# Performance work log

Measured on AMD Instinct MI355X. Metric: run time of the kernel, lower is better.

## Reference

```python
import jax, jax.numpy as jnp
import numpy as np

N = 80000      # nodes (spots)
D = 1000       # input_dim (genes)
E = 1280000    # edges (avg degree 16)
FH1, FH2 = 64, 16
GH1, GH2 = 64, 16
K = 10         # dec_cluster_n
ALPHA = 1.0
MASK = int(0.8 * N)
BN_EPS = 1e-3


def _xavier(key, shape):
    fan_in, fan_out = shape[0], shape[1]
    lim = jnp.sqrt(6.0 / (fan_in + fan_out))
    return jax.random.uniform(key, shape, jnp.float32, -lim, lim)


def setup_inputs() -> dict:
    key = jax.random.key(0)
    ks = jax.random.split(key, 32)
    x = jax.random.normal(ks[0], (N, D), jnp.float32)
    edge_rows = jax.random.randint(ks[1], (E,), 0, N, jnp.int32)
    edge_cols = jax.random.randint(ks[2], (E,), 0, N, jnp.int32)
    edge_vals = jax.random.uniform(ks[3], (E,), jnp.float32)
    mask_nodes = jax.random.permutation(ks[4], N)[:MASK].astype(jnp.int32)
    enc_mask_token = 0.02 * jax.random.normal(ks[5], (1, D), jnp.float32)
    # encoder L1: Linear + BatchNorm (eval: running stats)
    W1 = _xavier(ks[6], (D, FH1)); b1 = jnp.zeros((FH1,), jnp.float32)
    g1 = jnp.ones((FH1,), jnp.float32); be1 = jnp.zeros((FH1,), jnp.float32)
    rm1 = 0.1 * jax.random.normal(ks[7], (FH1,), jnp.float32)
    rv1 = 0.5 + jax.random.uniform(ks[8], (FH1,), jnp.float32)
    # encoder L2
    W2 = _xavier(ks[9], (FH1, FH2)); b2 = jnp.zeros((FH2,), jnp.float32)
    g2 = jnp.ones((FH2,), jnp.float32); be2 = jnp.zeros((FH2,), jnp.float32)
    rm2 = 0.1 * jax.random.normal(ks[10], (FH2,), jnp.float32)
    rv2 = 0.5 + jax.random.uniform(ks[11], (FH2,), jnp.float32)
    # GCN weights
    Wgc1 = _xavier(ks[12], (FH2, GH1))
    Wgc2 = _xavier(ks[13], (GH1, GH2))
    Wgc3 = _xavier(ks[14], (GH1, GH2))
    Wdec = _xavier(ks[15], (GH2 + FH2, D))
    cluster_layer = jax.random.normal(ks[16], (K, GH2 + FH2), jnp.float32) * jnp.sqrt(2.0 / (K + GH2 + FH2))
    return dict(x=x, edge_rows=edge_rows, edge_cols=edge_cols, edge_vals=edge_vals,
                mask_nodes=mask_nodes, enc_mask_token=enc_mask_token,
                W1=W1, b1=b1, g1=g1, be1=be1, rm1=rm1, rv1=rv1,
                W2=W2, b2=b2, g2=g2, be2=be2, rm2=rm2, rv2=rv2,
                Wgc1=Wgc1, Wgc2=Wgc2, Wgc3=Wgc3, Wdec=Wdec,
                cluster_layer=cluster_layer)


def _bn_eval(h, g, b, rm, rv):
    return (h - rm) * (g * jax.lax.rsqrt(rv + BN_EPS)) + b


def _spmm(rows, cols, vals, dense):
    # sparse adj [N,N] @ dense [N,F]
    return jax.ops.segment_sum(vals[:, None] * dense[cols], rows, num_segments=N)


def _l2norm(v):
    n = jnp.sqrt(jnp.sum(v * v, axis=-1, keepdims=True))
    return v / jnp.maximum(n, 1e-12)


def reference(x, edge_rows, edge_cols, edge_vals, mask_nodes, enc_mask_token,
              W1, b1, g1, be1, rm1, rv1, W2, b2, g2, be2, rm2, rv2,
              Wgc1, Wgc2, Wgc3, Wdec, cluster_layer):
    # encoding_mask_noise: add mask token to masked nodes (eval: dropout off)
    out_x = x.at[mask_nodes].add(enc_mask_token[0])
    # dense encoder (Linear -> BN(eval) -> ELU; dropout off)
    h = jax.nn.elu(_bn_eval(out_x @ W1 + b1, g1, be1, rm1, rv1))
    feat_x = jax.nn.elu(_bn_eval(h @ W2 + b2, g2, be2, rm2, rv2))
    # GCN layers: mm then spmm
    hidden1 = jax.nn.relu(_spmm(edge_rows, edge_cols, edge_vals, feat_x @ Wgc1))
    mu = _spmm(edge_rows, edge_cols, edge_vals, hidden1 @ Wgc2)
    logvar = _spmm(edge_rows, edge_cols, edge_vals, hidden1 @ Wgc3)
    gnn_z = mu  # eval-mode reparameterize
    z = jnp.concatenate([feat_x, gnn_z], axis=1)  # [N, 32]
    de_feat = _spmm(edge_rows, edge_cols, edge_vals, z @ Wdec)  # identity act
    # student-t cluster soft assignments
    d2 = jnp.sum(jnp.square(z[:, None, :] - cluster_layer[None, :, :]), axis=2)  # [N,K]
    q = 1.0 / (1.0 + d2 / ALPHA)
    q = q ** ((ALPHA + 1.0) / 2.0)
    q = q / jnp.sum(q, axis=1, keepdims=True)
    # sce loss on masked nodes
    x_init = out_x[mask_nodes]
    x_rec = de_feat[mask_nodes]
    loss = jnp.mean((1.0 - jnp.sum(_l2norm(x_rec) * _l2norm(x_init), axis=-1)) ** 3)
    return (z, mu, logvar, de_feat, q, feat_x, gnn_z, loss)
```

## Files before the change

kernel.cpp:

```cpp
#include <hip/hip_runtime.h>
#include <hip/hip_bf16.h>
#include <math.h>

#define Nn 80000
#define Dd 1000
#define Ee 1280000
#define MM 64000
#define NT 32

typedef __attribute__((ext_vector_type(8))) short bf16x8;
typedef __attribute__((ext_vector_type(4))) float f32x4;

__device__ inline unsigned short f2bf(float f){
  union { float f; unsigned u; } c; c.f = f;
  unsigned u = c.u;
  u += 0x7FFFu + ((u >> 16) & 1u);
  return (unsigned short)(u >> 16);
}
__device__ inline float bf2f(unsigned short s){
  return __uint_as_float(((unsigned)s) << 16);
}

__device__ __forceinline__ void gload16(const void* g, void* l){
  __builtin_amdgcn_global_load_lds(
      (const __attribute__((address_space(1))) void*)g,
      (__attribute__((address_space(3))) void*)l, 16, 0, 0);
}

__device__ __forceinline__ bf16x8 cvt8(f32x4 a, f32x4 b){
  union { __hip_bfloat162 h; unsigned u; } c0, c1, c2, c3;
  c0.h = __float22bfloat162_rn(make_float2(a.x, a.y));
  c1.h = __float22bfloat162_rn(make_float2(a.z, a.w));
  c2.h = __float22bfloat162_rn(make_float2(b.x, b.y));
  c3.h = __float22bfloat162_rn(make_float2(b.z, b.w));
  union { unsigned u[4]; bf16x8 v; } r;
  r.u[0] = c0.u; r.u[1] = c1.u; r.u[2] = c2.u; r.u[3] = c3.u;
  return r.v;
}

__global__ __launch_bounds__(256) void k_init(const float* __restrict__ W1,
    const float* __restrict__ Wdec, const float* __restrict__ token,
    unsigned short* __restrict__ Wim, unsigned short* __restrict__ WdT2,
    float* __restrict__ tw, int* __restrict__ flags, int* __restrict__ deg,
    float* __restrict__ loss)
{
  int i = blockIdx.x*256 + threadIdx.x;
  if (i < 131072){
    int t   = i >> 12;
    int rem = i & 4095;
    int c   = rem >> 5;
    int pos = rem & 31;
    int slot = pos >> 3;
    int j    = pos & 7;
    int u    = slot ^ (c & 3);
    int k    = t*32 + u*8 + j;
    float v = 0.f;
    if (c < 96 && k < Dd) v = (c < 64) ? W1[k*64 + c] : Wdec[(size_t)(c-64)*Dd + k];
    Wim[i] = f2bf(v);
  }
  unsigned t1 = (unsigned)(i - 131072);
  if (t1 < 32768u){
    int col = t1 >> 5, k = t1 & 31;
    WdT2[t1] = (col < Dd) ? f2bf(Wdec[(size_t)k*Dd + col]) : (unsigned short)0;
  }
  if (i < Nn){ flags[i] = 0; deg[i] = 0; }
  if (i == 0) *loss = 0.f;
  unsigned u3 = (unsigned)(i - 163840);
  if (u3 < 6208u){
    int j = u3 >> 6, l = u3 & 63;
    float s = 0.f;
    if (j < 64){ for (int k = l; k < Dd; k += 64) s += token[k]*W1[k*64 + j]; }
    else if (j < 96){ const float* wr = Wdec + (size_t)(j-64)*Dd;
                      for (int k = l; k < Dd; k += 64) s += token[k]*wr[k]; }
    else { for (int k = l; k < Dd; k += 64) s += token[k]*token[k]; }
    #pragma unroll
    for (int o = 32; o; o >>= 1) s += __shfl_down(s, o);
    if (l == 0) tw[j] = s;
  }
}

__global__ __launch_bounds__(256) void k_fillb(const int* __restrict__ rows,
    const int* __restrict__ cols, const float* __restrict__ vals,
    const int* __restrict__ mask, int* __restrict__ flags,
    int* __restrict__ deg, int2* __restrict__ buck, int lo, int hi)
{
  int i = blockIdx.x*256 + threadIdx.x;
  if (lo == 0 && i < MM) flags[mask[i]] = 1;
  if (i < Ee){
    int r = rows[i];
    if (r >= lo && r < hi){
      int s = atomicAdd(&deg[r], 1);
      if (s < 64){
        int2 pr; pr.x = cols[i]; pr.y = __float_as_int(vals[i]);
        buck[((size_t)r << 6) + s] = pr;
      }
    }
  }
}

__global__ __launch_bounds__(256, 3) void k_gemm1(
    const float* __restrict__ x, const unsigned short* __restrict__ Wim,
    const int* __restrict__ flags, const float* __restrict__ tw,
    const float* __restrict__ token,
    const float* __restrict__ b1, const float* __restrict__ g1,
    const float* __restrict__ be1, const float* __restrict__ rm1,
    const float* __restrict__ rv1, const float* __restrict__ W2,
    const float* __restrict__ b2, const float* __restrict__ g2,
    const float* __restrict__ be2, const float* __restrict__ rm2,
    const float* __restrict__ rv2, float* __restrict__ fx,
    float* __restrict__ wx, float* __restrict__ sii_node)
{
  __shared__ char smem[53248];
  float* tokL = (float*)(smem + 49152);
  const int tid  = threadIdx.x;
  const int lane = tid & 63;
  const int wave = tid >> 6;
  const int wm = wave >> 1, wn = wave & 1;
  const int l15 = lane & 15, kg = lane >> 4;
  const int swz = l15 & 7;
  const int row0 = blockIdx.x * 128;

  for (int i = tid; i < 1024; i += 256) tokL[i] = (i < Dd) ? token[i] : 0.f;
  __syncthreads();

  auto stage = [&](int t, char* Ab, char* Bb){
    int k0 = t*32;
    #pragma unroll
    for (int j = 0; j < 4; ++j){
      int s = (wave*4 + j)*64 + lane;
      int r = s >> 3, u = s & 7;
      int col = k0 + ((u ^ (r & 7)) << 2);
      if (col > 996) col = 996;
      gload16(x + (size_t)(row0 + r)*Dd + col, Ab + (wave*4 + j)*1024);
    }
    const char* wim = (const char*)Wim + (size_t)t*8192;
    #pragma unroll
    for (int j = 0; j < 2; ++j){
      int ch = wave*2 + j;
      gload16(wim + ch*1024 + lane*16, Bb + ch*1024);
    }
  };

  stage(0, smem,         smem + 32768);
  stage(1, smem + 16384, smem + 40960);

  const f32x4 zero4 = {0.f,0.f,0.f,0.f};
  f32x4 acc[4][3];
  #pragma unroll
  for (int i = 0; i < 4; ++i){ acc[i][0]=zero4; acc[i][1]=zero4; acc[i][2]=zero4; }
  float sx2[4] = {0.f,0.f,0.f,0.f};
  float sxt[4] = {0.f,0.f,0.f,0.f};

  #pragma unroll 2
  for (int t = 0; t < NT; ++t){
    if (t < NT-1) asm volatile("s_waitcnt vmcnt(6)" ::: "memory");
    else          asm volatile("s_waitcnt vmcnt(0)" ::: "memory");
    __builtin_amdgcn_s_barrier();
    __builtin_amdgcn_sched_barrier(0);

    const char* Ab = smem + (t&1)*16384;
    const char* Bb = smem + 32768 + (t&1)*8192;
    const int k0 = t*32;

    f32x4 tk0 = *(const f32x4*)(tokL + k0 + kg*8);
    f32x4 tk1 = *(const f32x4*)(tokL + k0 + kg*8 + 4);

    bf16x8 bfr[3];
    #pragma unroll
    for (int ni = 0; ni < 3; ++ni){
      int c = wn*48 + ni*16 + l15;
      bfr[ni] = *(const bf16x8*)(Bb + c*64 + ((kg ^ (c & 3)) << 4));
    }
    bool kv = (k0 + kg*8) <= 992;
    #pragma unroll
    for (int mi = 0; mi < 4; ++mi){
      int r = wm*64 + mi*16 + l15;
      f32x4 xa = *(const f32x4*)(Ab + r*128 + (((2*kg  ) ^ swz) << 4));
      f32x4 xb = *(const f32x4*)(Ab + r*128 + (((2*kg+1) ^ swz) << 4));
      if (wn == 0 && kv){
        sx2[mi] += xa.x*xa.x + xa.y*xa.y + xa.z*xa.z + xa.w*xa.w
                 + xb.x*xb.x + xb.y*xb.y + xb.z*xb.z + xb.w*xb.w;
        sxt[mi] += xa.x*tk0.x + xa.y*tk0.y + xa.z*tk0.z + xa.w*tk0.w
                 + xb.x*tk1.x + xb.y*tk1.y + xb.z*tk1.z + xb.w*tk1.w;
      }
      bf16x8 af = cvt8(xa, xb);
      acc[mi][0] = __builtin_amdgcn_mfma_f32_16x16x32_bf16(af, bfr[0], acc[mi][0], 0, 0, 0);
      acc[mi][1] = __builtin_amdgcn_mfma_f32_16x16x32_bf16(af, bfr[1], acc[mi][1], 0, 0, 0);
      acc[mi][2] = __builtin_amdgcn_mfma_f32_16x16x32_bf16(af, bfr[2], acc[mi][2], 0, 0, 0);
    }

    __builtin_amdgcn_sched_barrier(0);
    __builtin_amdgcn_s_barrier();
    if (t + 2 < NT)
      stage(t+2, smem + (t&1)*16384, smem + 32768 + (t&1)*8192);
  }

  float stt = tw[96];
  if (wn == 0){
    #pragma unroll
    for (int mi = 0; mi < 4; ++mi){
      float a2 = sx2[mi]; a2 += __shfl_xor(a2, 16); a2 += __shfl_xor(a2, 32);
      float at = sxt[mi]; at += __shfl_xor(at, 16); at += __shfl_xor(at, 32);
      if (lane < 16){
        int row = row0 + wm*64 + mi*16 + lane;
        float fl = flags[row] ? 1.f : 0.f;
        sii_node[row] = a2 + fl*(2.f*at + stt);
      }
    }
  }

  float flv[4][4];
  #pragma unroll
  for (int mi = 0; mi < 4; ++mi)
    #pragma unroll
    for (int r4 = 0; r4 < 4; ++r4)
      flv[mi][r4] = flags[row0 + wm*64 + mi*16 + (lane>>4)*4 + r4] ? 1.f : 0.f;

  float* Hs  = (float*)smem;
  float* W2s = (float*)(smem + 36864);
  for (int i = tid; i < 1024; i += 256) W2s[i] = W2[i];

  #pragma unroll
  for (int ni = 0; ni < 3; ++ni){
    int n = wn*48 + ni*16 + l15;
    float twn = tw[n];
    if (n < 64){
      float bb = b1[n], rmv = rm1[n];
      float scv = g1[n]*rsqrtf(rv1[n] + 1e-3f), bev = be1[n];
      #pragma unroll
      for (int mi = 0; mi < 4; ++mi){
        #pragma unroll
        for (int r4 = 0; r4 < 4; ++r4){
          int lrow = wm*64 + mi*16 + (lane>>4)*4 + r4;
          float v = (acc[mi][ni][r4] + flv[mi][r4]*twn + bb - rmv)*scv + bev;
          v = (v > 0.f) ? v : expm1f(v);
          Hs[lrow*66 + n] = v;
        }
      }
    } else {
      int j = n - 64;
      #pragma unroll
      for (int mi = 0; mi < 4; ++mi){
        #pragma unroll
        for (int r4 = 0; r4 < 4; ++r4){
          int lrow = wm*64 + mi*16 + (lane>>4)*4 + r4;
          wx[(size_t)(row0 + lrow)*32 + j] = acc[mi][ni][r4] + flv[mi][r4]*twn;
        }
      }
    }
  }
  __syncthreads();

  {
    int j = tid & 15;
    float pb = b2[j], prm = rm2[j];
    float psc = g2[j]*rsqrtf(rv2[j] + 1e-3f), pbe = be2[j];
    int rb = (tid >> 4) * 8;
    #pragma unroll
    for (int rr = 0; rr < 8; ++rr){
      int r = rb + rr;
      float a = pb;
      #pragma unroll
      for (int k = 0; k < 64; ++k) a += Hs[r*66 + k]*W2s[k*16 + j];
      float v = (a - prm)*psc + pbe;
      v = (v > 0.f) ? v : expm1f(v);
      fx[(size_t)(row0 + r)*16 + j] = v;
    }
  }
}

template<bool WITH_H1>
__global__ __launch_bounds__(256) void k_spmm16(const int* __restrict__ deg,
    const int2* __restrict__ buck, const float* __restrict__ in,
    float* __restrict__ out, const float* __restrict__ Wgc1,
    unsigned short* __restrict__ h1b)
{
  __shared__ float Ws[1024];
  if (WITH_H1){
    for (int t = threadIdx.x; t < 1024; t += 256) Ws[t] = Wgc1[t];
    __syncthreads();
  }
  int row = blockIdx.x*16 + (threadIdx.x >> 4);
  int l = threadIdx.x & 15;
  int d = deg[row]; if (d > 64) d = 64;
  const int2* bp = buck + ((size_t)row << 6);
  float acc = 0.f;
  for (int p = 0; p < d; ++p){
    int2 ce = bp[p];
    acc += __int_as_float(ce.y) * in[(size_t)ce.x*16 + l];
  }
  out[(size_t)row*16 + l] = acc;
  if (WITH_H1){
    float h0=0.f, h1=0.f, h2=0.f, h3=0.f;
    #pragma unroll
    for (int k = 0; k < 16; ++k){
      float av = __shfl(acc, k, 16);
      const float* wp = &Ws[k*64 + l*4];
      h0 += av*wp[0]; h1 += av*wp[1]; h2 += av*wp[2]; h3 += av*wp[3];
    }
    ushort4 pk;
    pk.x = f2bf(fmaxf(h0, 0.f)); pk.y = f2bf(fmaxf(h1, 0.f));
    pk.z = f2bf(fmaxf(h2, 0.f)); pk.w = f2bf(fmaxf(h3, 0.f));
    *reinterpret_cast<ushort4*>(&h1b[(size_t)row*64 + l*4]) = pk;
  }
}

__global__ __launch_bounds__(256) void k_gcn2(const int* __restrict__ deg,
    const int2* __restrict__ buck, const unsigned short* __restrict__ h1b,
    const float* __restrict__ Wgc2, const float* __restrict__ Wgc3,
    const float* __restrict__ fx, const float* __restrict__ cl,
    float* __restrict__ z, float* __restrict__ mu,
    float* __restrict__ lv, float* __restrict__ gz, float* __restrict__ q)
{
  __shared__ float ah[16][65];
  __shared__ float Ws[2048];
  __shared__ float cls[320];
  __shared__ float zs[16][33];
  __shared__ float qv[16][10];
  int t = threadIdx.x;
  for (int i = t; i < 1024; i += 256){ Ws[i] = Wgc2[i]; Ws[1024 + i] = Wgc3[i]; }
  for (int i = t; i < 320; i += 256) cls[i] = cl[i];
  const int wave = t >> 6, lane = t & 63;
  const int row0 = blockIdx.x*16;
  #pragma unroll
  for (int rr = 0; rr < 4; ++rr){
    int lr = wave*4 + rr;
    int row = row0 + lr;
    int d = deg[row]; if (d > 64) d = 64;
    const int2* bp = buck + ((size_t)row << 6);
    float acc = 0.f;
    for (int p = 0; p < d; ++p){
      int2 ce = bp[p];
      acc += __int_as_float(ce.y) * bf2f(h1b[(size_t)ce.x*64 + lane]);
    }
    ah[lr][lane] = acc;
  }
  __syncthreads();
  {
    int r = t >> 4, j = t & 15;
    const float* ar = ah[r];
    float m = 0.f, l = 0.f;
    #pragma unroll 16
    for (int k = 0; k < 64; ++k){
      float a = ar[k];
      m += a*Ws[k*16 + j];
      l += a*Ws[1024 + k*16 + j];
    }
    size_t grow = (size_t)(row0 + r);
    mu[grow*16 + j] = m;
    gz[grow*16 + j] = m;
    z[grow*32 + 16 + j] = m;
    zs[r][16 + j] = m;
    lv[grow*16 + j] = l;
    float v = fx[grow*16 + j];
    z[grow*32 + j] = v;
    zs[r][j] = v;
  }
  __syncthreads();
  if (t < 160){
    int r = t / 10, c = t - r*10;
    float d2 = 0.f;
    #pragma unroll
    for (int k = 0; k < 32; ++k){ float d = zs[r][k] - cls[c*32 + k]; d2 += d*d; }
    qv[r][c] = 1.f/(1.f + d2);
  }
  __syncthreads();
  if (t < 160){
    int r = t / 10, c = t - r*10;
    float ss = 0.f;
    #pragma unroll
    for (int cc = 0; cc < 10; ++cc) ss += qv[r][cc];
    q[(size_t)(row0 + r)*10 + c] = qv[r][c]/ss;
  }
}

__global__ __launch_bounds__(256) void k_dec(const float* __restrict__ afx,
    const float* __restrict__ amu, const unsigned short* __restrict__ WdT2,
    const float* __restrict__ wx, const float* __restrict__ sii_node,
    const int* __restrict__ flags, float* __restrict__ de,
    float* __restrict__ loss)
{
  __shared__ float stg[4][16][68];
  __shared__ float bsum[4];
  const int lane = threadIdx.x & 63;
  const int wave = threadIdx.x >> 6;
  const int r0 = blockIdx.x*64 + wave*16;
  const int kg = lane >> 4;
  const int l15 = lane & 15;
  const int row = r0 + l15;
  const float* asrc = (kg < 2) ? (afx + (size_t)row*16 + kg*8)
                               : (amu + (size_t)row*16 + (kg-2)*8);
  f32x4 a0 = *reinterpret_cast<const f32x4*>(asrc);
  f32x4 a1 = *reinterpret_cast<const f32x4*>(asrc + 4);
  bf16x8 af = cvt8(a0, a1);
  const float* wsrc = wx + (size_t)row*32 + kg*8;
  f32x4 w0 = *reinterpret_cast<const f32x4*>(wsrc);
  f32x4 w1 = *reinterpret_cast<const f32x4*>(wsrc + 4);
  float sri = a0.x*w0.x + a0.y*w0.y + a0.z*w0.z + a0.w*w0.w
            + a1.x*w1.x + a1.y*w1.y + a1.z*w1.z + a1.w*w1.w;

  const f32x4 zero4 = {0.f,0.f,0.f,0.f};
  float sq = 0.f;
  float (*S)[68] = stg[wave];
  const int srow = lane >> 4;
  const int scol = l15*4;

  for (int g = 0; g < 16; ++g){
    int c0 = g*64;
    #pragma unroll
    for (int j = 0; j < 4; ++j){
      int cb = c0 + j*16;
      bf16x8 bf = *reinterpret_cast<const bf16x8*>(&WdT2[(size_t)(cb + l15)*32 + kg*8]);
      f32x4 d = __builtin_amdgcn_mfma_f32_16x16x32_bf16(bf, af, zero4, 0, 0, 0);
      sq += d[0]*d[0] + d[1]*d[1] + d[2]*d[2] + d[3]*d[3];
      *reinterpret_cast<f32x4*>(&S[l15][j*16 + kg*4]) = d;
    }
    asm volatile("s_waitcnt lgkmcnt(0)" ::: "memory");
    __builtin_amdgcn_sched_barrier(0);
    #pragma unroll
    for (int sub = 0; sub < 4; ++sub){
      int lr = sub*4 + srow;
      int cc = c0 + scol;
      if (cc < Dd){
        f32x4 v = *reinterpret_cast<const f32x4*>(&S[lr][scol]);
        *reinterpret_cast<f32x4*>(&de[(size_t)(r0 + lr)*Dd + cc]) = v;
      }
    }
    __builtin_amdgcn_sched_barrier(0);
    asm volatile("s_waitcnt lgkmcnt(0)" ::: "memory");
  }
  sq  += __shfl_xor(sq, 16);  sq  += __shfl_xor(sq, 32);
  sri += __shfl_xor(sri, 16); sri += __shfl_xor(sri, 32);
  float tval = 0.f;
  if (kg == 0){
    float nr = fmaxf(sqrtf(sq), 1e-12f);
    float ni = fmaxf(sqrtf(sii_node[row]), 1e-12f);
    float tt = 1.f - sri/(nr*ni);
    tval = flags[row] ? tt*tt*tt : 0.f;
  }
  #pragma unroll
  for (int o = 1; o < 16; o <<= 1) tval += __shfl_xor(tval, o);
  if (lane == 0) bsum[wave] = tval;
  __syncthreads();
  if (threadIdx.x == 0)
    atomicAdd(loss, (bsum[0] + bsum[1] + bsum[2] + bsum[3]) * (1.f/MM));
}

extern "C" void kernel_launch(void* const* d_in, const int* in_sizes, int n_in,
                              void* d_out, int out_size, void* d_ws, size_t ws_size,
                              hipStream_t stream)
{
  const float* x     = (const float*)d_in[0];
  const int*   erow  = (const int*)  d_in[1];
  const int*   ecol  = (const int*)  d_in[2];
  const float* evls  = (const float*)d_in[3];
  const int*   mask  = (const int*)  d_in[4];
  const float* token = (const float*)d_in[5];
  const float* W1  = (const float*)d_in[6];
  const float* b1  = (const float*)d_in[7];
  const float* g1  = (const float*)d_in[8];
  const float* be1 = (const float*)d_in[9];
  const float* rm1 = (const float*)d_in[10];
  const float* rv1 = (const float*)d_in[11];
  const float* W2  = (const float*)d_in[12];
  const float* b2  = (const float*)d_in[13];
  const float* g2  = (const float*)d_in[14];
  const float* be2 = (const float*)d_in[15];
  const float* rm2 = (const float*)d_in[16];
  const float* rv2 = (const float*)d_in[17];
  const float* Wgc1= (const float*)d_in[18];
  const float* Wgc2= (const float*)d_in[19];
  const float* Wgc3= (const float*)d_in[20];
  const float* Wdec= (const float*)d_in[21];
  const float* clus= (const float*)d_in[22];

  float* out = (float*)d_out;
  float* oz  = out;
  float* omu = out + (size_t)Nn*32;
  float* olv = omu + (size_t)Nn*16;
  float* ode = olv + (size_t)Nn*16;
  float* oq  = ode + (size_t)Nn*1000;
  float* ofx = oq  + (size_t)Nn*10;
  float* ogz = ofx + (size_t)Nn*16;
  float* olo = ogz + (size_t)Nn*16;

  char* w = (char*)d_ws;
  unsigned short* Wim  = (unsigned short*)w; w += (size_t)262144;
  unsigned short* WdT2 = (unsigned short*)w; w += (size_t)65536;
  float* tw    = (float*)w; w += 512;
  int* flags   = (int*)w;   w += (size_t)Nn*4;
  int* deg     = (int*)w;   w += (size_t)Nn*4;
  int2* buck   = (int2*)w;  w += (size_t)Nn*64*8;
  float* afx   = (float*)w; w += (size_t)Nn*16*4;
  float* amu   = (float*)w; w += (size_t)Nn*16*4;
  unsigned short* h1b = (unsigned short*)w; w += (size_t)Nn*64*2;
  float* wx    = (float*)w; w += (size_t)Nn*32*4;
  float* sii   = (float*)w; w += (size_t)Nn*4;

  k_init<<<dim3(665), dim3(256), 0, stream>>>(W1, Wdec, token, Wim, WdT2, tw,
      flags, deg, olo);
  k_fillb<<<dim3((Ee+255)/256), dim3(256), 0, stream>>>(erow, ecol, evls, mask,
      flags, deg, buck, 0, 40000);
  k_fillb<<<dim3((Ee+255)/256), dim3(256), 0, stream>>>(erow, ecol, evls, mask,
      flags, deg, buck, 40000, 80000);
  k_gemm1<<<dim3(Nn/128), dim3(256), 0, stream>>>(x, Wim, flags, tw, token,
      b1, g1, be1, rm1, rv1, W2, b2, g2, be2, rm2, rv2, ofx, wx, sii);
  k_spmm16<true><<<dim3(Nn/16), dim3(256), 0, stream>>>(deg, buck, ofx, afx, Wgc1, h1b);
  k_gcn2<<<dim3(Nn/16), dim3(256), 0, stream>>>(deg, buck, h1b, Wgc2, Wgc3,
      ofx, clus, oz, omu, olv, ogz, oq);
  k_spmm16<false><<<dim3(Nn/16), dim3(256), 0, stream>>>(deg, buck, omu, amu, nullptr, nullptr);
  k_dec<<<dim3(Nn/64), dim3(256), 0, stream>>>(afx, amu, WdT2, wx, sii, flags, ode, olo);
}
```

Before: 544.3 us.

## Fuse edge bucketing into GEMM1 launch and fold mu SpMM into decoder

Removes the two row-range-split bucket-fill launches. Edge bucketing now runs as extra blocks (index 625 and up) of the k_gemm1 grid, so the atomic scatter overlaps the dense encoder GEMM. The third SpMM over mu is computed inside k_dec into shared memory, which drops one launch and the amu round trip through global memory. The trade-offs are a much larger gemm1 grid with mixed block types, heavier shared-memory use in k_dec, and loss of the row-range split that may have been chosen for atomic or cache locality.

```diff
diff --git a/kernel.cpp b/kernel.cpp
--- a/kernel.cpp
+++ b/kernel.cpp
@@ -79,23 +79,11 @@
   }
 }
 
-__global__ __launch_bounds__(256) void k_fillb(const int* __restrict__ rows,
-    const int* __restrict__ cols, const float* __restrict__ vals,
-    const int* __restrict__ mask, int* __restrict__ flags,
-    int* __restrict__ deg, int2* __restrict__ buck, int lo, int hi)
+__global__ __launch_bounds__(256) void k_flags(const int* __restrict__ mask,
+    int* __restrict__ flags)
 {
   int i = blockIdx.x*256 + threadIdx.x;
-  if (lo == 0 && i < MM) flags[mask[i]] = 1;
-  if (i < Ee){
-    int r = rows[i];
-    if (r >= lo && r < hi){
-      int s = atomicAdd(&deg[r], 1);
-      if (s < 64){
-        int2 pr; pr.x = cols[i]; pr.y = __float_as_int(vals[i]);
-        buck[((size_t)r << 6) + s] = pr;
-      }
-    }
-  }
+  if (i < MM) flags[mask[i]] = 1;
 }
 
 __global__ __launch_bounds__(256, 3) void k_gemm1(
@@ -108,9 +96,24 @@
     const float* __restrict__ b2, const float* __restrict__ g2,
     const float* __restrict__ be2, const float* __restrict__ rm2,
     const float* __restrict__ rv2, float* __restrict__ fx,
-    float* __restrict__ wx, float* __restrict__ sii_node)
+    float* __restrict__ wx, float* __restrict__ sii_node,
+    const int* __restrict__ erow, const int* __restrict__ ecol,
+    const float* __restrict__ evls, int* __restrict__ deg,
+    int2* __restrict__ buck)
 {
   __shared__ char smem[53248];
+  if (blockIdx.x >= 625){
+    int i = (blockIdx.x - 625)*256 + threadIdx.x;
+    if (i < Ee){
+      int r = erow[i];
+      int s = atomicAdd(&deg[r], 1);
+      if (s < 64){
+        int2 pr; pr.x = ecol[i]; pr.y = __float_as_int(evls[i]);
+        buck[((size_t)r << 6) + s] = pr;
+      }
+    }
+    return;
+  }
   float* tokL = (float*)(smem + 49152);
   const int tid  = threadIdx.x;
   const int lane = tid & 63;
@@ -269,17 +272,14 @@
   }
 }
 
-template<bool WITH_H1>
 __global__ __launch_bounds__(256) void k_spmm16(const int* __restrict__ deg,
     const int2* __restrict__ buck, const float* __restrict__ in,
     float* __restrict__ out, const float* __restrict__ Wgc1,
     unsigned short* __restrict__ h1b)
 {
   __shared__ float Ws[1024];
-  if (WITH_H1){
-    for (int t = threadIdx.x; t < 1024; t += 256) Ws[t] = Wgc1[t];
-    __syncthreads();
-  }
+  for (int t = threadIdx.x; t < 1024; t += 256) Ws[t] = Wgc1[t];
+  __syncthreads();
   int row = blockIdx.x*16 + (threadIdx.x >> 4);
   int l = threadIdx.x & 15;
   int d = deg[row]; if (d > 64) d = 64;
@@ -290,19 +290,17 @@
     acc += __int_as_float(ce.y) * in[(size_t)ce.x*16 + l];
   }
   out[(size_t)row*16 + l] = acc;
-  if (WITH_H1){
-    float h0=0.f, h1=0.f, h2=0.f, h3=0.f;
-    #pragma unroll
-    for (int k = 0; k < 16; ++k){
-      float av = __shfl(acc, k, 16);
-      const float* wp = &Ws[k*64 + l*4];
-      h0 += av*wp[0]; h1 += av*wp[1]; h2 += av*wp[2]; h3 += av*wp[3];
-    }
-    ushort4 pk;
-    pk.x = f2bf(fmaxf(h0, 0.f)); pk.y = f2bf(fmaxf(h1, 0.f));
-    pk.z = f2bf(fmaxf(h2, 0.f)); pk.w = f2bf(fmaxf(h3, 0.f));
-    *reinterpret_cast<ushort4*>(&h1b[(size_t)row*64 + l*4]) = pk;
-  }
+  float h0=0.f, h1=0.f, h2=0.f, h3=0.f;
+  #pragma unroll
+  for (int k = 0; k < 16; ++k){
+    float av = __shfl(acc, k, 16);
+    const float* wp = &Ws[k*64 + l*4];
+    h0 += av*wp[0]; h1 += av*wp[1]; h2 += av*wp[2]; h3 += av*wp[3];
+  }
+  ushort4 pk;
+  pk.x = f2bf(fmaxf(h0, 0.f)); pk.y = f2bf(fmaxf(h1, 0.f));
+  pk.z = f2bf(fmaxf(h2, 0.f)); pk.w = f2bf(fmaxf(h3, 0.f));
+  *reinterpret_cast<ushort4*>(&h1b[(size_t)row*64 + l*4]) = pk;
 }
 
 __global__ __launch_bounds__(256) void k_gcn2(const int* __restrict__ deg,
@@ -375,23 +373,52 @@
 }
 
 __global__ __launch_bounds__(256) void k_dec(const float* __restrict__ afx,
-    const float* __restrict__ amu, const unsigned short* __restrict__ WdT2,
+    const float* __restrict__ mu, const int* __restrict__ deg,
+    const int2* __restrict__ buck, const unsigned short* __restrict__ WdT2,
     const float* __restrict__ wx, const float* __restrict__ sii_node,
     const int* __restrict__ flags, float* __restrict__ de,
     float* __restrict__ loss)
 {
   __shared__ float stg[4][16][68];
+  __shared__ float amuL[64][17];
   __shared__ float bsum[4];
-  const int lane = threadIdx.x & 63;
-  const int wave = threadIdx.x >> 6;
-  const int r0 = blockIdx.x*64 + wave*16;
+  const int tid  = threadIdx.x;
+  const int lane = tid & 63;
+  const int wave = tid >> 6;
+  const int base = blockIdx.x*64;
+
+  {
+    int l = tid & 15, rg = tid >> 4;
+    #pragma unroll
+    for (int pass = 0; pass < 4; ++pass){
+      int lr = pass*16 + rg;
+      int row = base + lr;
+      int d = deg[row]; if (d > 64) d = 64;
+      const int2* bp = buck + ((size_t)row << 6);
+      float acc = 0.f;
+      for (int p = 0; p < d; ++p){
+        int2 ce = bp[p];
+        acc += __int_as_float(ce.y) * mu[(size_t)ce.x*16 + l];
+      }
+      amuL[lr][l] = acc;
+    }
+  }
+  __syncthreads();
+
+  const int r0 = base + wave*16;
   const int kg = lane >> 4;
   const int l15 = lane & 15;
   const int row = r0 + l15;
-  const float* asrc = (kg < 2) ? (afx + (size_t)row*16 + kg*8)
-                               : (amu + (size_t)row*16 + (kg-2)*8);
-  f32x4 a0 = *reinterpret_cast<const f32x4*>(asrc);
-  f32x4 a1 = *reinterpret_cast<const f32x4*>(asrc + 4);
+  f32x4 a0, a1;
+  if (kg < 2){
+    const float* asrc = afx + (size_t)row*16 + kg*8;
+    a0 = *reinterpret_cast<const f32x4*>(asrc);
+    a1 = *reinterpret_cast<const f32x4*>(asrc + 4);
+  } else {
+    const float* asrc = &amuL[wave*16 + l15][(kg-2)*8];
+    a0 = *reinterpret_cast<const f32x4*>(asrc);
+    a1 = *reinterpret_cast<const f32x4*>(asrc + 4);
+  }
   bf16x8 af = cvt8(a0, a1);
   const float* wsrc = wx + (size_t)row*32 + kg*8;
   f32x4 w0 = *reinterpret_cast<const f32x4*>(wsrc);
@@ -442,7 +469,7 @@
   for (int o = 1; o < 16; o <<= 1) tval += __shfl_xor(tval, o);
   if (lane == 0) bsum[wave] = tval;
   __syncthreads();
-  if (threadIdx.x == 0)
+  if (tid == 0)
     atomicAdd(loss, (bsum[0] + bsum[1] + bsum[2] + bsum[3]) * (1.f/MM));
 }
 
@@ -492,22 +519,19 @@
   int* deg     = (int*)w;   w += (size_t)Nn*4;
   int2* buck   = (int2*)w;  w += (size_t)Nn*64*8;
   float* afx   = (float*)w; w += (size_t)Nn*16*4;
-  float* amu   = (float*)w; w += (size_t)Nn*16*4;
   unsigned short* h1b = (unsigned short*)w; w += (size_t)Nn*64*2;
   float* wx    = (float*)w; w += (size_t)Nn*32*4;
   float* sii   = (float*)w; w += (size_t)Nn*4;
 
   k_init<<<dim3(665), dim3(256), 0, stream>>>(W1, Wdec, token, Wim, WdT2, tw,
       flags, deg, olo);
-  k_fillb<<<dim3((Ee+255)/256), dim3(256), 0, stream>>>(erow, ecol, evls, mask,
-      flags, deg, buck, 0, 40000);
-  k_fillb<<<dim3((Ee+255)/256), dim3(256), 0, stream>>>(erow, ecol, evls, mask,
-      flags, deg, buck, 40000, 80000);
-  k_gemm1<<<dim3(Nn/128), dim3(256), 0, stream>>>(x, Wim, flags, tw, token,
-      b1, g1, be1, rm1, rv1, W2, b2, g2, be2, rm2, rv2, ofx, wx, sii);
-  k_spmm16<true><<<dim3(Nn/16), dim3(256), 0, stream>>>(deg, buck, ofx, afx, Wgc1, h1b);
+  k_flags<<<dim3((MM+255)/256), dim3(256), 0, stream>>>(mask, flags);
+  k_gemm1<<<dim3(5625), dim3(256), 0, stream>>>(x, Wim, flags, tw, token,
+      b1, g1, be1, rm1, rv1, W2, b2, g2, be2, rm2, rv2, ofx, wx, sii,
+      erow, ecol, evls, deg, buck);
+  k_spmm16<<<dim3(Nn/16), dim3(256), 0, stream>>>(deg, buck, ofx, afx, Wgc1, h1b);
   k_gcn2<<<dim3(Nn/16), dim3(256), 0, stream>>>(deg, buck, h1b, Wgc2, Wgc3,
       ofx, clus, oz, omu, olv, ogz, oq);
-  k_spmm16<false><<<dim3(Nn/16), dim3(256), 0, stream>>>(deg, buck, omu, amu, nullptr, nullptr);
-  k_dec<<<dim3(Nn/64), dim3(256), 0, stream>>>(afx, amu, WdT2, wx, sii, flags, ode, olo);
-}
+  k_dec<<<dim3(Nn/64), dim3(256), 0, stream>>>(afx, omu, deg, buck, WdT2,
+      wx, sii, flags, ode, olo);
+}
```

After: 489.7 us. 10.0% less time.
